# Performance work log

Measured on AMD Instinct MI355X. Metric: run time of the kernel, lower is better.

The kernel has to match this reference:

```python
import jax, jax.numpy as jnp
import numpy as np

N_IN, N_OUT, D_H = 128, 128, 1024
EPS = 1e-5

def _bn(x, g, b):
    # BatchNorm1d in training mode: per-batch mean / biased variance
    m = jnp.mean(x, axis=0)
    v = jnp.mean((x - m) ** 2, axis=0)
    return g * (x - m) / jnp.sqrt(v + EPS) + b

def setup_inputs() -> dict:
    key = jax.random.key(0)
    ks = jax.random.split(key, 16)
    d_comb = N_IN + D_H
    s1 = 1.0 / np.sqrt(d_comb)
    s2 = 1.0 / np.sqrt(D_H)
    return {
        "X": jax.random.normal(ks[0], (512, 256, N_IN), dtype=jnp.float32),
        "W_u": jax.random.uniform(ks[1], (D_H, d_comb), jnp.float32, -s1, s1),
        "b_u": jax.random.uniform(ks[2], (D_H,), jnp.float32, -s1, s1),
        "W_r": jax.random.uniform(ks[3], (D_H, d_comb), jnp.float32, -s1, s1),
        "b_r": jax.random.uniform(ks[4], (D_H,), jnp.float32, -s1, s1),
        "W_h": jax.random.uniform(ks[5], (D_H, d_comb), jnp.float32, -s1, s1),
        "b_h": jax.random.uniform(ks[6], (D_H,), jnp.float32, -s1, s1),
        "W_o": jax.random.uniform(ks[7], (N_OUT, D_H), jnp.float32, -s2, s2),
        "b_o": jax.random.uniform(ks[8], (N_OUT,), jnp.float32, -s2, s2),
        "g_u": jnp.ones((D_H,), jnp.float32), "be_u": jnp.zeros((D_H,), jnp.float32),
        "g_r": jnp.ones((D_H,), jnp.float32), "be_r": jnp.zeros((D_H,), jnp.float32),
        "g_h": jnp.ones((D_H,), jnp.float32), "be_h": jnp.zeros((D_H,), jnp.float32),
    }

def reference(X, W_u, b_u, W_r, b_r, W_h, b_h, W_o, b_o,
              g_u, be_u, g_r, be_r, g_h, be_h):
    # X: (B, S, n_inputs); dropout p=0 -> identity
    B = X.shape[0]
    Xs = jnp.transpose(X, (1, 0, 2))  # (S, B, n_in)

    def step(h, x):
        comb = jnp.concatenate([x, h], axis=-1)                 # (B, n_in+d_h)
        u = jax.nn.sigmoid(_bn(comb @ W_u.T + b_u, g_u, be_u))  # update gate
        r = jax.nn.sigmoid(_bn(comb @ W_r.T + b_r, g_r, be_r))  # reset gate
        comb2 = jnp.concatenate([x, r * h], axis=-1)
        c = jnp.tanh(_bn(comb2 @ W_h.T + b_h, g_h, be_h))       # candidate
        h_new = (1.0 - u) * c + u * h
        o = jnp.tanh(h_new @ W_o.T + b_o)
        return h_new, o

    h0 = jnp.zeros((B, D_H), dtype=X.dtype)
    _, out = jax.lax.scan(step, h0, Xs)      # out: (S, B, n_out)
    return jnp.transpose(out, (1, 0, 2))     # (B, S, n_out)
```

## Files before the change

### kernel.cpp

```cpp
#include <hip/hip_runtime.h>

#define BB   512
#define SS   256
#define NIN  128
#define DH   1024
#define DC   1152
#define NOUT 128
#define EPSV 1e-5f

typedef _Float16 f16;
typedef _Float16 f16x8 __attribute__((ext_vector_type(8)));
typedef _Float16 f16x4 __attribute__((ext_vector_type(4)));
typedef float    f32x4 __attribute__((ext_vector_type(4)));

__device__ __forceinline__ float sigmoid_(float x) { return 1.0f / (1.0f + __expf(-x)); }
__device__ __forceinline__ float tanh_(float x) {
    x = fminf(fmaxf(x, -15.0f), 15.0f);
    float e = __expf(2.0f * x);
    return (e - 1.0f) / (e + 1.0f);
}

__global__ void k_convert(const float* __restrict__ Wu, const float* __restrict__ Wr,
                          const float* __restrict__ Wh_, const float* __restrict__ Wo_,
                          f16* __restrict__ wur, f16* __restrict__ wh, f16* __restrict__ wo)
{
    const int stride = gridDim.x * blockDim.x;
    const int i0 = blockIdx.x * blockDim.x + threadIdx.x;
    for (int i = i0; i < 2048 * 1152 / 4; i += stride) {
        int base = i * 4;
        int n = base / 1152, k = base % 1152;
        const float* src = (n < 1024) ? (Wu + (size_t)n * 1152 + k) : (Wr + (size_t)(n - 1024) * 1152 + k);
        float4 v = *(const float4*)src;
        f16x4 o; o[0] = (f16)v.x; o[1] = (f16)v.y; o[2] = (f16)v.z; o[3] = (f16)v.w;
        *(f16x4*)(wur + base) = o;
    }
    for (int i = i0; i < 1024 * 1152 / 4; i += stride) {
        int base = i * 4;
        float4 v = *(const float4*)(Wh_ + base);
        f16x4 o; o[0] = (f16)v.x; o[1] = (f16)v.y; o[2] = (f16)v.z; o[3] = (f16)v.w;
        *(f16x4*)(wh + base) = o;
    }
    for (int i = i0; i < 128 * 1024 / 4; i += stride) {
        int base = i * 4;
        float4 v = *(const float4*)(Wo_ + base);
        f16x4 o; o[0] = (f16)v.x; o[1] = (f16)v.y; o[2] = (f16)v.z; o[3] = (f16)v.w;
        *(f16x4*)(wo + base) = o;
    }
}

__global__ void k_init(const float* __restrict__ X, f16* __restrict__ comb, float* __restrict__ h32,
                       float* __restrict__ ssum_ur, float* __restrict__ ssq_ur,
                       float* __restrict__ ssum_c, float* __restrict__ ssq_c)
{
    const int stride = gridDim.x * blockDim.x;
    const int i0 = blockIdx.x * blockDim.x + threadIdx.x;
    for (int i = i0; i < BB * DC / 4; i += stride) {
        int base = i * 4;
        int m = base / DC, k = base % DC;
        f16x4 o;
        if (k < NIN) {
            float4 v = *(const float4*)(X + (size_t)m * SS * NIN + k);
            o[0] = (f16)v.x; o[1] = (f16)v.y; o[2] = (f16)v.z; o[3] = (f16)v.w;
        } else {
            o[0] = (f16)0.f; o[1] = (f16)0.f; o[2] = (f16)0.f; o[3] = (f16)0.f;
        }
        *(f16x4*)(comb + base) = o;
    }
    for (int i = i0; i < BB * DH / 4; i += stride)
        *(float4*)(h32 + i * 4) = make_float4(0.f, 0.f, 0.f, 0.f);
    for (int i = i0; i < 2 * 2048; i += stride) { ssum_ur[i] = 0.f; ssq_ur[i] = 0.f; }
    for (int i = i0; i < 2 * 1024; i += stride) { ssum_c[i] = 0.f; ssq_c[i] = 0.f; }
}

template<int KT, bool OEPI>
__device__ __forceinline__ void gemm_job(
    const f16* __restrict__ A, int lda, const f16* __restrict__ Bm,
    float* __restrict__ C, int ldc,
    float* __restrict__ ssum, float* __restrict__ ssq,
    const float* __restrict__ bo, float* __restrict__ outp, int so,
    int m0, int n0, f16 (*As)[64][72], f16 (*Bs)[64][72])
{
    constexpr int KH = KT / 2;
    constexpr int NC = KH / 64;
    const int tid  = threadIdx.x;
    const int lane = tid & 63;
    const int wave = tid >> 6;
    const int g    = tid >> 8;
    const int sq   = wave & 3, wm = sq >> 1, wn = sq & 1;
    const int t    = tid & 255;
    const int r0   = t >> 3, kg = t & 7;

    const f16* Ap  = A  + (size_t)(m0 + r0) * lda + g * KH + kg * 8;
    const f16* Ap2 = Ap + (size_t)32 * lda;
    const f16* Bp  = Bm + (size_t)(n0 + r0) * KT + g * KH + kg * 8;
    const f16* Bp2 = Bp + (size_t)32 * KT;

    f32x4 acc[2][2] = {};
    f16x8 pa0 = *(const f16x8*)Ap;
    f16x8 pa1 = *(const f16x8*)Ap2;
    f16x8 pb0 = *(const f16x8*)Bp;
    f16x8 pb1 = *(const f16x8*)Bp2;

    for (int c = 0; c < NC; ++c) {
        *(f16x8*)&As[g][r0][kg * 8]      = pa0;
        *(f16x8*)&As[g][r0 + 32][kg * 8] = pa1;
        *(f16x8*)&Bs[g][r0][kg * 8]      = pb0;
        *(f16x8*)&Bs[g][r0 + 32][kg * 8] = pb1;
        __syncthreads();
        if (c + 1 < NC) {
            pa0 = *(const f16x8*)(Ap  + (c + 1) * 64);
            pa1 = *(const f16x8*)(Ap2 + (c + 1) * 64);
            pb0 = *(const f16x8*)(Bp  + (c + 1) * 64);
            pb1 = *(const f16x8*)(Bp2 + (c + 1) * 64);
        }
#pragma unroll
        for (int ks = 0; ks < 2; ++ks) {
            const int kofs = ks * 32 + (lane >> 4) * 8;
            f16x8 a0 = *(const f16x8*)&As[g][wm * 32 + (lane & 15)][kofs];
            f16x8 a1 = *(const f16x8*)&As[g][wm * 32 + 16 + (lane & 15)][kofs];
            f16x8 b0 = *(const f16x8*)&Bs[g][wn * 32 + (lane & 15)][kofs];
            f16x8 b1 = *(const f16x8*)&Bs[g][wn * 32 + 16 + (lane & 15)][kofs];
            acc[0][0] = __builtin_amdgcn_mfma_f32_16x16x32_f16(a0, b0, acc[0][0], 0, 0, 0);
            acc[0][1] = __builtin_amdgcn_mfma_f32_16x16x32_f16(a0, b1, acc[0][1], 0, 0, 0);
            acc[1][0] = __builtin_amdgcn_mfma_f32_16x16x32_f16(a1, b0, acc[1][0], 0, 0, 0);
            acc[1][1] = __builtin_amdgcn_mfma_f32_16x16x32_f16(a1, b1, acc[1][1], 0, 0, 0);
        }
        __syncthreads();
    }

    float* red = (float*)As;
    const int rbase = (sq * 64 + lane) * 20;
    if (g == 1) {
#pragma unroll
        for (int fm = 0; fm < 2; ++fm)
#pragma unroll
            for (int fn = 0; fn < 2; ++fn)
                *(f32x4*)&red[rbase + (fm * 2 + fn) * 4] = acc[fm][fn];
    }
    __syncthreads();
    if (g == 0) {
#pragma unroll
        for (int fm = 0; fm < 2; ++fm)
#pragma unroll
            for (int fn = 0; fn < 2; ++fn)
                acc[fm][fn] += *(const f32x4*)&red[rbase + (fm * 2 + fn) * 4];

#pragma unroll
        for (int fm = 0; fm < 2; ++fm) {
#pragma unroll
            for (int fn = 0; fn < 2; ++fn) {
                const int row = m0 + wm * 32 + fm * 16 + (lane >> 4) * 4;
                const int col = n0 + wn * 32 + fn * 16 + (lane & 15);
                if constexpr (OEPI) {
#pragma unroll
                    for (int i = 0; i < 4; ++i) {
                        float v = tanh_(acc[fm][fn][i] + bo[col]);
                        outp[(size_t)(row + i) * (SS * NOUT) + (size_t)so * NOUT + col] = v;
                    }
                } else {
#pragma unroll
                    for (int i = 0; i < 4; ++i)
                        C[(size_t)(row + i) * ldc + col] = acc[fm][fn][i];
                }
            }
        }
        if constexpr (!OEPI) {
#pragma unroll
            for (int fn = 0; fn < 2; ++fn) {
                float s1 = 0.f, s2 = 0.f;
#pragma unroll
                for (int fm = 0; fm < 2; ++fm)
#pragma unroll
                    for (int i = 0; i < 4; ++i) { float v = acc[fm][fn][i]; s1 += v; s2 += v * v; }
                s1 += __shfl_xor(s1, 16, 64); s1 += __shfl_xor(s1, 32, 64);
                s2 += __shfl_xor(s2, 16, 64); s2 += __shfl_xor(s2, 32, 64);
                if (lane < 16) {
                    const int col = n0 + wn * 32 + fn * 16 + lane;
                    atomicAdd(&ssum[col], s1);
                    atomicAdd(&ssq[col], s2);
                }
            }
        }
    }
}

__global__ __launch_bounds__(512, 4)
void k_uro(const f16* __restrict__ comb, const f16* __restrict__ Wur, const f16* __restrict__ Wo16,
           float* __restrict__ pre_ur,
           float* __restrict__ ssum, float* __restrict__ ssq,
           const float* __restrict__ b_o, float* __restrict__ outp, int s)
{
    __shared__ __align__(16) f16 smem[2][2][64][72];
    const int b = blockIdx.x;
    if (b < 16) {
        if (s == 0) return;
        const int m0 = (b >> 1) * 64, n0 = (b & 1) * 64;
        gemm_job<DH, true>(comb + NIN, DC, Wo16, nullptr, 0, nullptr, nullptr,
                           b_o, outp, s - 1, m0, n0, smem[0], smem[1]);
    } else {
        const int j = b - 16;
        const int m0 = (j >> 5) * 64, n0 = (j & 31) * 64;
        gemm_job<DC, false>(comb, DC, Wur, pre_ur, 2048, ssum, ssq,
                            nullptr, nullptr, 0, m0, n0, smem[0], smem[1]);
    }
}

__global__ __launch_bounds__(512, 4)
void k_c8(const f16* __restrict__ comb, const f16* __restrict__ Wh16,
          float* __restrict__ pre_c, float* __restrict__ ssum, float* __restrict__ ssq)
{
    __shared__ __align__(16) f16 smem[2][2][64][72];
    const int b = blockIdx.x;
    const int m0 = (b >> 4) * 64, n0 = (b & 15) * 64;
    gemm_job<DC, false>(comb, DC, Wh16, pre_c, 1024, ssum, ssq,
                        nullptr, nullptr, 0, m0, n0, smem[0], smem[1]);
}

__global__ __launch_bounds__(512, 4)
void k_o16(const f16* __restrict__ comb, const f16* __restrict__ Wo16,
           const float* __restrict__ b_o, float* __restrict__ outp)
{
    __shared__ __align__(16) f16 smem[2][2][64][72];
    const int b = blockIdx.x;
    const int m0 = (b >> 1) * 64, n0 = (b & 1) * 64;
    gemm_job<DH, true>(comb + NIN, DC, Wo16, nullptr, 0, nullptr, nullptr,
                       b_o, outp, SS - 1, m0, n0, smem[0], smem[1]);
}

__global__ __launch_bounds__(256)
void k_gate(const float* __restrict__ pre_ur, const float* __restrict__ h32,
            f16* __restrict__ comb,
            const float* __restrict__ ssum_ur, const float* __restrict__ ssq_ur,
            const float* __restrict__ g_r, const float* __restrict__ be_r)
{
    const int idx = blockIdx.x * 256 + threadIdx.x;
    const int m = idx >> 8, j4 = (idx & 255) << 2;
    float4 prv = *(const float4*)(pre_ur + (size_t)m * 2048 + 1024 + j4);
    float4 hv  = *(const float4*)(h32 + (size_t)m * 1024 + j4);
    float p[4] = {prv.x, prv.y, prv.z, prv.w};
    float h[4] = {hv.x, hv.y, hv.z, hv.w};
    f16x4 o;
#pragma unroll
    for (int t = 0; t < 4; ++t) {
        const int col = 1024 + j4 + t;
        float mu  = ssum_ur[col] * (1.0f / 512.0f);
        float var = fmaxf(ssq_ur[col] * (1.0f / 512.0f) - mu * mu, 0.f);
        float r   = sigmoid_(g_r[j4 + t] * ((p[t] - mu) * rsqrtf(var + EPSV)) + be_r[j4 + t]);
        o[t] = (f16)(r * h[t]);
    }
    *(f16x4*)(comb + (size_t)m * DC + NIN + j4) = o;
}

__global__ __launch_bounds__(256)
void k_upd(const float* __restrict__ pre_ur, const float* __restrict__ pre_c,
           float* __restrict__ h32, f16* __restrict__ comb,
           const float* __restrict__ ssum_ur, const float* __restrict__ ssq_ur,
           const float* __restrict__ ssum_c, const float* __restrict__ ssq_c,
           float* __restrict__ zsum_ur, float* __restrict__ zsq_ur,
           float* __restrict__ zsum_c, float* __restrict__ zsq_c,
           const float* __restrict__ X,
           const float* __restrict__ g_u, const float* __restrict__ be_u,
           const float* __restrict__ g_h, const float* __restrict__ be_h,
           int s)
{
    const int idx = blockIdx.x * 256 + threadIdx.x;
    const int m = idx >> 8, j4 = (idx & 255) << 2;
    float4 puv = *(const float4*)(pre_ur + (size_t)m * 2048 + j4);
    float4 pcv = *(const float4*)(pre_c + (size_t)m * 1024 + j4);
    float4 hv  = *(const float4*)(h32 + (size_t)m * 1024 + j4);
    float pu[4] = {puv.x, puv.y, puv.z, puv.w};
    float pc[4] = {pcv.x, pcv.y, pcv.z, pcv.w};
    float h[4]  = {hv.x, hv.y, hv.z, hv.w};
    float hn[4];
    f16x4 o;
#pragma unroll
    for (int t = 0; t < 4; ++t) {
        const int col = j4 + t;
        float mu_u  = ssum_ur[col] * (1.0f / 512.0f);
        float var_u = fmaxf(ssq_ur[col] * (1.0f / 512.0f) - mu_u * mu_u, 0.f);
        float u = sigmoid_(g_u[col] * ((pu[t] - mu_u) * rsqrtf(var_u + EPSV)) + be_u[col]);
        float mu_c  = ssum_c[col] * (1.0f / 512.0f);
        float var_c = fmaxf(ssq_c[col] * (1.0f / 512.0f) - mu_c * mu_c, 0.f);
        float c = tanh_(g_h[col] * ((pc[t] - mu_c) * rsqrtf(var_c + EPSV)) + be_h[col]);
        float hnew = (1.f - u) * c + u * h[t];
        hn[t] = hnew; o[t] = (f16)hnew;
    }
    *(float4*)(h32 + (size_t)m * 1024 + j4) = make_float4(hn[0], hn[1], hn[2], hn[3]);
    *(f16x4*)(comb + (size_t)m * DC + NIN + j4) = o;
    if (j4 < NIN && s + 1 < SS) {
        float4 xv = *(const float4*)(X + (size_t)m * SS * NIN + (size_t)(s + 1) * NIN + j4);
        f16x4 xo; xo[0] = (f16)xv.x; xo[1] = (f16)xv.y; xo[2] = (f16)xv.z; xo[3] = (f16)xv.w;
        *(f16x4*)(comb + (size_t)m * DC + j4) = xo;
    }
    if (idx < 2048) { zsum_ur[idx] = 0.f; zsq_ur[idx] = 0.f; }
    if (idx < 1024) { zsum_c[idx] = 0.f; zsq_c[idx] = 0.f; }
}

extern "C" void kernel_launch(void* const* d_in, const int* in_sizes, int n_in,
                              void* d_out, int out_size, void* d_ws, size_t ws_size,
                              hipStream_t stream)
{
    const float* X    = (const float*)d_in[0];
    const float* W_u  = (const float*)d_in[1];
    const float* W_r  = (const float*)d_in[3];
    const float* W_h  = (const float*)d_in[5];
    const float* W_o  = (const float*)d_in[7];
    const float* b_o  = (const float*)d_in[8];
    const float* g_u  = (const float*)d_in[9];
    const float* be_u = (const float*)d_in[10];
    const float* g_r  = (const float*)d_in[11];
    const float* be_r = (const float*)d_in[12];
    const float* g_h  = (const float*)d_in[13];
    const float* be_h = (const float*)d_in[14];
    float* out = (float*)d_out;

    char* p = (char*)d_ws;
    auto alloc = [&](size_t bytes) { char* r = p; p += (bytes + 255) & ~(size_t)255; return r; };
    f16*   comb    = (f16*)alloc((size_t)BB * DC * 2);
    f16*   Wur     = (f16*)alloc((size_t)2048 * DC * 2);
    f16*   Wh16    = (f16*)alloc((size_t)DH * DC * 2);
    f16*   Wo16    = (f16*)alloc((size_t)NOUT * DH * 2);
    float* pre_ur  = (float*)alloc((size_t)BB * 2048 * 4);
    float* pre_c   = (float*)alloc((size_t)BB * DH * 4);
    float* h32     = (float*)alloc((size_t)BB * DH * 4);
    float* ssum_ur = (float*)alloc(2 * 2048 * 4);
    float* ssq_ur  = (float*)alloc(2 * 2048 * 4);
    float* ssum_c  = (float*)alloc(2 * 1024 * 4);
    float* ssq_c   = (float*)alloc(2 * 1024 * 4);

    k_convert<<<1024, 256, 0, stream>>>(W_u, W_r, W_h, W_o, Wur, Wh16, Wo16);
    k_init<<<1024, 256, 0, stream>>>(X, comb, h32, ssum_ur, ssq_ur, ssum_c, ssq_c);

    for (int s = 0; s < SS; ++s) {
        const int par = s & 1, nxt = 1 - par;
        k_uro<<<272, 512, 0, stream>>>(comb, Wur, Wo16, pre_ur,
                                       ssum_ur + par * 2048, ssq_ur + par * 2048,
                                       b_o, out, s);
        k_gate<<<512, 256, 0, stream>>>(pre_ur, h32, comb,
            ssum_ur + par * 2048, ssq_ur + par * 2048, g_r, be_r);
        k_c8<<<128, 512, 0, stream>>>(comb, Wh16, pre_c,
                                      ssum_c + par * 1024, ssq_c + par * 1024);
        k_upd<<<512, 256, 0, stream>>>(pre_ur, pre_c, h32, comb,
            ssum_ur + par * 2048, ssq_ur + par * 2048,
            ssum_c + par * 1024, ssq_c + par * 1024,
            ssum_ur + nxt * 2048, ssq_ur + nxt * 2048,
            ssum_c + nxt * 1024, ssq_c + nxt * 1024,
            X, g_u, be_u, g_h, be_h, s);
    }
    k_o16<<<16, 512, 0, stream>>>(comb, Wo16, b_o, out);
}
```

Measured before the change: 8.055 ms.

## Fuse reset-gate computation into candidate GEMM A-tile loading and regroup kernels

Removes the separate reset-gate elementwise kernel. The candidate GEMM now builds its A operand on the fly from pre_ur, h32 and the BN statistics, computing sigmoid(r)*h directly into shared memory. The output projection moves from the update/reset GEMM launch into the candidate GEMM launch, and launch bounds drop from 4 to 2 blocks per CU. This saves one launch per timestep plus the f16 write and re-read of the gated half of comb. In exchange, each of the 16 column blocks recomputes the gate for its rows and reads fp32 pre_ur and h32 instead of f16, which adds redundant transcendental work and extra memory traffic.

```diff
diff --git a/kernel.cpp b/kernel.cpp
--- a/kernel.cpp
+++ b/kernel.cpp
@@ -184,39 +184,165 @@
     }
 }
 
-__global__ __launch_bounds__(512, 4)
-void k_uro(const f16* __restrict__ comb, const f16* __restrict__ Wur, const f16* __restrict__ Wo16,
-           float* __restrict__ pre_ur,
-           float* __restrict__ ssum, float* __restrict__ ssq,
-           const float* __restrict__ b_o, float* __restrict__ outp, int s)
+__device__ __forceinline__ void gemm_job_cgate(
+    const f16* __restrict__ comb, const float* __restrict__ pre_ur, const float* __restrict__ h32,
+    const float* __restrict__ su, const float* __restrict__ qu,
+    const float* __restrict__ g_r, const float* __restrict__ be_r,
+    const f16* __restrict__ Bm,
+    float* __restrict__ C, int ldc,
+    float* __restrict__ ssum, float* __restrict__ ssq,
+    int m0, int n0, f16 (*As)[64][72], f16 (*Bs)[64][72])
+{
+    constexpr int KT = DC, KH = KT / 2, NC = KH / 64;
+    const int tid  = threadIdx.x;
+    const int lane = tid & 63;
+    const int wave = tid >> 6;
+    const int g    = tid >> 8;
+    const int sq   = wave & 3, wm = sq >> 1, wn = sq & 1;
+    const int t    = tid & 255;
+    const int r0   = t >> 3, kg = t & 7;
+
+    const f16* Bp  = Bm + (size_t)(n0 + r0) * KT + g * KH + kg * 8;
+    const f16* Bp2 = Bp + (size_t)32 * KT;
+    const int kb   = g * KH + kg * 8;
+
+    f32x4 acc[2][2] = {};
+
+    for (int c = 0; c < NC; ++c) {
+        const int k8 = kb + c * 64;
+        f16x8 a0, a1;
+        if (k8 < NIN) {
+            a0 = *(const f16x8*)(comb + (size_t)(m0 + r0) * DC + k8);
+            a1 = *(const f16x8*)(comb + (size_t)(m0 + r0 + 32) * DC + k8);
+        } else {
+            const int j = k8 - NIN;
+            float sc[8], bi[8];
+#pragma unroll
+            for (int q = 0; q < 8; ++q) {
+                float mu  = su[1024 + j + q] * (1.0f / 512.0f);
+                float var = fmaxf(qu[1024 + j + q] * (1.0f / 512.0f) - mu * mu, 0.f);
+                float a   = g_r[j + q] * rsqrtf(var + EPSV);
+                sc[q] = a; bi[q] = be_r[j + q] - a * mu;
+            }
+            const float* pr0 = pre_ur + (size_t)(m0 + r0) * 2048 + 1024 + j;
+            const float* pr1 = pre_ur + (size_t)(m0 + r0 + 32) * 2048 + 1024 + j;
+            const float* hr0 = h32 + (size_t)(m0 + r0) * 1024 + j;
+            const float* hr1 = h32 + (size_t)(m0 + r0 + 32) * 1024 + j;
+            f32x4 p00 = *(const f32x4*)pr0, p01 = *(const f32x4*)(pr0 + 4);
+            f32x4 p10 = *(const f32x4*)pr1, p11 = *(const f32x4*)(pr1 + 4);
+            f32x4 h00 = *(const f32x4*)hr0, h01 = *(const f32x4*)(hr0 + 4);
+            f32x4 h10 = *(const f32x4*)hr1, h11 = *(const f32x4*)(hr1 + 4);
+#pragma unroll
+            for (int q = 0; q < 4; ++q) {
+                a0[q]     = (f16)(sigmoid_(sc[q] * p00[q] + bi[q]) * h00[q]);
+                a0[q + 4] = (f16)(sigmoid_(sc[q + 4] * p01[q] + bi[q + 4]) * h01[q]);
+                a1[q]     = (f16)(sigmoid_(sc[q] * p10[q] + bi[q]) * h10[q]);
+                a1[q + 4] = (f16)(sigmoid_(sc[q + 4] * p11[q] + bi[q + 4]) * h11[q]);
+            }
+        }
+        f16x8 b0v = *(const f16x8*)(Bp  + c * 64);
+        f16x8 b1v = *(const f16x8*)(Bp2 + c * 64);
+        *(f16x8*)&As[g][r0][kg * 8]      = a0;
+        *(f16x8*)&As[g][r0 + 32][kg * 8] = a1;
+        *(f16x8*)&Bs[g][r0][kg * 8]      = b0v;
+        *(f16x8*)&Bs[g][r0 + 32][kg * 8] = b1v;
+        __syncthreads();
+#pragma unroll
+        for (int ks = 0; ks < 2; ++ks) {
+            const int kofs = ks * 32 + (lane >> 4) * 8;
+            f16x8 fa0 = *(const f16x8*)&As[g][wm * 32 + (lane & 15)][kofs];
+            f16x8 fa1 = *(const f16x8*)&As[g][wm * 32 + 16 + (lane & 15)][kofs];
+            f16x8 fb0 = *(const f16x8*)&Bs[g][wn * 32 + (lane & 15)][kofs];
+            f16x8 fb1 = *(const f16x8*)&Bs[g][wn * 32 + 16 + (lane & 15)][kofs];
+            acc[0][0] = __builtin_amdgcn_mfma_f32_16x16x32_f16(fa0, fb0, acc[0][0], 0, 0, 0);
+            acc[0][1] = __builtin_amdgcn_mfma_f32_16x16x32_f16(fa0, fb1, acc[0][1], 0, 0, 0);
+            acc[1][0] = __builtin_amdgcn_mfma_f32_16x16x32_f16(fa1, fb0, acc[1][0], 0, 0, 0);
+            acc[1][1] = __builtin_amdgcn_mfma_f32_16x16x32_f16(fa1, fb1, acc[1][1], 0, 0, 0);
+        }
+        __syncthreads();
+    }
+
+    float* red = (float*)As;
+    const int rbase = (sq * 64 + lane) * 20;
+    if (g == 1) {
+#pragma unroll
+        for (int fm = 0; fm < 2; ++fm)
+#pragma unroll
+            for (int fn = 0; fn < 2; ++fn)
+                *(f32x4*)&red[rbase + (fm * 2 + fn) * 4] = acc[fm][fn];
+    }
+    __syncthreads();
+    if (g == 0) {
+#pragma unroll
+        for (int fm = 0; fm < 2; ++fm)
+#pragma unroll
+            for (int fn = 0; fn < 2; ++fn)
+                acc[fm][fn] += *(const f32x4*)&red[rbase + (fm * 2 + fn) * 4];
+
+#pragma unroll
+        for (int fm = 0; fm < 2; ++fm)
+#pragma unroll
+            for (int fn = 0; fn < 2; ++fn) {
+                const int row = m0 + wm * 32 + fm * 16 + (lane >> 4) * 4;
+                const int col = n0 + wn * 32 + fn * 16 + (lane & 15);
+#pragma unroll
+                for (int i = 0; i < 4; ++i)
+                    C[(size_t)(row + i) * ldc + col] = acc[fm][fn][i];
+            }
+#pragma unroll
+        for (int fn = 0; fn < 2; ++fn) {
+            float s1 = 0.f, s2 = 0.f;
+#pragma unroll
+            for (int fm = 0; fm < 2; ++fm)
+#pragma unroll
+                for (int i = 0; i < 4; ++i) { float v = acc[fm][fn][i]; s1 += v; s2 += v * v; }
+            s1 += __shfl_xor(s1, 16, 64); s1 += __shfl_xor(s1, 32, 64);
+            s2 += __shfl_xor(s2, 16, 64); s2 += __shfl_xor(s2, 32, 64);
+            if (lane < 16) {
+                const int col = n0 + wn * 32 + fn * 16 + lane;
+                atomicAdd(&ssum[col], s1);
+                atomicAdd(&ssq[col], s2);
+            }
+        }
+    }
+}
+
+__global__ __launch_bounds__(512, 2)
+void k_ur(const f16* __restrict__ comb, const f16* __restrict__ Wur,
+          float* __restrict__ pre_ur, float* __restrict__ ssum, float* __restrict__ ssq)
 {
     __shared__ __align__(16) f16 smem[2][2][64][72];
     const int b = blockIdx.x;
-    if (b < 16) {
+    const int m0 = (b >> 5) * 64, n0 = (b & 31) * 64;
+    gemm_job<DC, false>(comb, DC, Wur, pre_ur, 2048, ssum, ssq,
+                        nullptr, nullptr, 0, m0, n0, smem[0], smem[1]);
+}
+
+__global__ __launch_bounds__(512, 2)
+void k_cgo(const f16* __restrict__ comb, const float* __restrict__ pre_ur, const float* __restrict__ h32,
+           const f16* __restrict__ Wh16, const f16* __restrict__ Wo16,
+           float* __restrict__ pre_c,
+           const float* __restrict__ su, const float* __restrict__ qu,
+           float* __restrict__ sc_, float* __restrict__ qc_,
+           const float* __restrict__ g_r, const float* __restrict__ be_r,
+           const float* __restrict__ b_o, float* __restrict__ outp, int s)
+{
+    __shared__ __align__(16) f16 smem[2][2][64][72];
+    const int b = blockIdx.x;
+    if (b < 128) {
+        const int m0 = (b >> 4) * 64, n0 = (b & 15) * 64;
+        gemm_job_cgate(comb, pre_ur, h32, su, qu, g_r, be_r, Wh16,
+                       pre_c, 1024, sc_, qc_, m0, n0, smem[0], smem[1]);
+    } else {
         if (s == 0) return;
-        const int m0 = (b >> 1) * 64, n0 = (b & 1) * 64;
+        const int j = b - 128;
+        const int m0 = (j >> 1) * 64, n0 = (j & 1) * 64;
         gemm_job<DH, true>(comb + NIN, DC, Wo16, nullptr, 0, nullptr, nullptr,
                            b_o, outp, s - 1, m0, n0, smem[0], smem[1]);
-    } else {
-        const int j = b - 16;
-        const int m0 = (j >> 5) * 64, n0 = (j & 31) * 64;
-        gemm_job<DC, false>(comb, DC, Wur, pre_ur, 2048, ssum, ssq,
-                            nullptr, nullptr, 0, m0, n0, smem[0], smem[1]);
-    }
-}
-
-__global__ __launch_bounds__(512, 4)
-void k_c8(const f16* __restrict__ comb, const f16* __restrict__ Wh16,
-          float* __restrict__ pre_c, float* __restrict__ ssum, float* __restrict__ ssq)
-{
-    __shared__ __align__(16) f16 smem[2][2][64][72];
-    const int b = blockIdx.x;
-    const int m0 = (b >> 4) * 64, n0 = (b & 15) * 64;
-    gemm_job<DC, false>(comb, DC, Wh16, pre_c, 1024, ssum, ssq,
-                        nullptr, nullptr, 0, m0, n0, smem[0], smem[1]);
-}
-
-__global__ __launch_bounds__(512, 4)
+    }
+}
+
+__global__ __launch_bounds__(512, 2)
 void k_o16(const f16* __restrict__ comb, const f16* __restrict__ Wo16,
            const float* __restrict__ b_o, float* __restrict__ outp)
 {
@@ -225,30 +351,6 @@
     const int m0 = (b >> 1) * 64, n0 = (b & 1) * 64;
     gemm_job<DH, true>(comb + NIN, DC, Wo16, nullptr, 0, nullptr, nullptr,
                        b_o, outp, SS - 1, m0, n0, smem[0], smem[1]);
-}
-
-__global__ __launch_bounds__(256)
-void k_gate(const float* __restrict__ pre_ur, const float* __restrict__ h32,
-            f16* __restrict__ comb,
-            const float* __restrict__ ssum_ur, const float* __restrict__ ssq_ur,
-            const float* __restrict__ g_r, const float* __restrict__ be_r)
-{
-    const int idx = blockIdx.x * 256 + threadIdx.x;
-    const int m = idx >> 8, j4 = (idx & 255) << 2;
-    float4 prv = *(const float4*)(pre_ur + (size_t)m * 2048 + 1024 + j4);
-    float4 hv  = *(const float4*)(h32 + (size_t)m * 1024 + j4);
-    float p[4] = {prv.x, prv.y, prv.z, prv.w};
-    float h[4] = {hv.x, hv.y, hv.z, hv.w};
-    f16x4 o;
-#pragma unroll
-    for (int t = 0; t < 4; ++t) {
-        const int col = 1024 + j4 + t;
-        float mu  = ssum_ur[col] * (1.0f / 512.0f);
-        float var = fmaxf(ssq_ur[col] * (1.0f / 512.0f) - mu * mu, 0.f);
-        float r   = sigmoid_(g_r[j4 + t] * ((p[t] - mu) * rsqrtf(var + EPSV)) + be_r[j4 + t]);
-        o[t] = (f16)(r * h[t]);
-    }
-    *(f16x4*)(comb + (size_t)m * DC + NIN + j4) = o;
 }
 
 __global__ __launch_bounds__(256)
@@ -333,13 +435,12 @@
 
     for (int s = 0; s < SS; ++s) {
         const int par = s & 1, nxt = 1 - par;
-        k_uro<<<272, 512, 0, stream>>>(comb, Wur, Wo16, pre_ur,
+        k_ur<<<256, 512, 0, stream>>>(comb, Wur, pre_ur,
+                                      ssum_ur + par * 2048, ssq_ur + par * 2048);
+        k_cgo<<<144, 512, 0, stream>>>(comb, pre_ur, h32, Wh16, Wo16, pre_c,
                                        ssum_ur + par * 2048, ssq_ur + par * 2048,
-                                       b_o, out, s);
-        k_gate<<<512, 256, 0, stream>>>(pre_ur, h32, comb,
-            ssum_ur + par * 2048, ssq_ur + par * 2048, g_r, be_r);
-        k_c8<<<128, 512, 0, stream>>>(comb, Wh16, pre_c,
-                                      ssum_c + par * 1024, ssq_c + par * 1024);
+                                       ssum_c + par * 1024, ssq_c + par * 1024,
+                                       g_r, be_r, b_o, out, s);
         k_upd<<<512, 256, 0, stream>>>(pre_ur, pre_c, h32, comb,
             ssum_ur + par * 2048, ssq_ur + par * 2048,
             ssum_c + par * 1024, ssq_c + par * 1024,
```

After: 10.52 ms. +30.6%, slower.

## Fuse gate and update elementwise kernels into GEMM tails via last-block counters

Applied to the files above, without the earlier changes.

Removes the separate k_gate and k_upd launches by having the last GEMM block finishing each 64-column group (detected with an atomic counter) apply the BatchNorm+activation epilogue for that column slice. The reset-gated hidden is written to a separate double-buffered comb buffer so the u/r/o GEMM and the candidate GEMM read consistent inputs. Per step this cuts kernel launches from four to two. In exchange it adds atomic counters, fences, and a serialized epilogue on one block per column group, and launch bounds drop to 2 waves per EU.

```diff
diff --git a/kernel.cpp b/kernel.cpp
--- a/kernel.cpp
+++ b/kernel.cpp
@@ -48,9 +48,11 @@
     }
 }
 
-__global__ void k_init(const float* __restrict__ X, f16* __restrict__ comb, float* __restrict__ h32,
+__global__ void k_init(const float* __restrict__ X, f16* __restrict__ combA, f16* __restrict__ combB,
+                       float* __restrict__ h32,
                        float* __restrict__ ssum_ur, float* __restrict__ ssq_ur,
-                       float* __restrict__ ssum_c, float* __restrict__ ssq_c)
+                       float* __restrict__ ssum_c, float* __restrict__ ssq_c,
+                       unsigned* __restrict__ urt, unsigned* __restrict__ ct)
 {
     const int stride = gridDim.x * blockDim.x;
     const int i0 = blockIdx.x * blockDim.x + threadIdx.x;
@@ -64,12 +66,16 @@
         } else {
             o[0] = (f16)0.f; o[1] = (f16)0.f; o[2] = (f16)0.f; o[3] = (f16)0.f;
         }
-        *(f16x4*)(comb + base) = o;
+        *(f16x4*)(combA + base) = o;
+        *(f16x4*)(combB + base) = o;
+        f16x4 z; z[0] = (f16)0.f; z[1] = (f16)0.f; z[2] = (f16)0.f; z[3] = (f16)0.f;
+        *(f16x4*)(combB + (size_t)BB * DC + base) = z;
     }
     for (int i = i0; i < BB * DH / 4; i += stride)
         *(float4*)(h32 + i * 4) = make_float4(0.f, 0.f, 0.f, 0.f);
     for (int i = i0; i < 2 * 2048; i += stride) { ssum_ur[i] = 0.f; ssq_ur[i] = 0.f; }
     for (int i = i0; i < 2 * 1024; i += stride) { ssum_c[i] = 0.f; ssq_c[i] = 0.f; }
+    for (int i = i0; i < 16; i += stride) { urt[i] = 0u; ct[i] = 0u; }
 }
 
 template<int KT, bool OEPI>
@@ -184,116 +190,152 @@
     }
 }
 
-__global__ __launch_bounds__(512, 4)
-void k_uro(const f16* __restrict__ comb, const f16* __restrict__ Wur, const f16* __restrict__ Wo16,
+__global__ __launch_bounds__(512, 2)
+void k_uro(const f16* __restrict__ combA, const f16* __restrict__ Wur, const f16* __restrict__ Wo16,
            float* __restrict__ pre_ur,
            float* __restrict__ ssum, float* __restrict__ ssq,
-           const float* __restrict__ b_o, float* __restrict__ outp, int s)
+           f16* __restrict__ combB_par, const float* __restrict__ h32,
+           const float* __restrict__ g_r, const float* __restrict__ be_r,
+           const float* __restrict__ b_o, float* __restrict__ outp,
+           unsigned* __restrict__ urt, int s)
 {
     __shared__ __align__(16) f16 smem[2][2][64][72];
+    __shared__ int lastFlag;
     const int b = blockIdx.x;
     if (b < 16) {
         if (s == 0) return;
         const int m0 = (b >> 1) * 64, n0 = (b & 1) * 64;
-        gemm_job<DH, true>(comb + NIN, DC, Wo16, nullptr, 0, nullptr, nullptr,
+        gemm_job<DH, true>(combA + NIN, DC, Wo16, nullptr, 0, nullptr, nullptr,
                            b_o, outp, s - 1, m0, n0, smem[0], smem[1]);
-    } else {
-        const int j = b - 16;
-        const int m0 = (j >> 5) * 64, n0 = (j & 31) * 64;
-        gemm_job<DC, false>(comb, DC, Wur, pre_ur, 2048, ssum, ssq,
-                            nullptr, nullptr, 0, m0, n0, smem[0], smem[1]);
-    }
-}
-
-__global__ __launch_bounds__(512, 4)
-void k_c8(const f16* __restrict__ comb, const f16* __restrict__ Wh16,
-          float* __restrict__ pre_c, float* __restrict__ ssum, float* __restrict__ ssq)
+        return;
+    }
+    const int j = b - 16;
+    const int m0 = (j >> 5) * 64, n0 = (j & 31) * 64;
+    gemm_job<DC, false>(combA, DC, Wur, pre_ur, 2048, ssum, ssq,
+                        nullptr, nullptr, 0, m0, n0, smem[0], smem[1]);
+    if (n0 < 1024) return;
+    const int gid = (n0 - 1024) >> 6;
+    __syncthreads();
+    if (threadIdx.x == 0) {
+        __threadfence();
+        unsigned n = __hip_atomic_fetch_add(&urt[gid], 1u, __ATOMIC_ACQ_REL, __HIP_MEMORY_SCOPE_AGENT);
+        lastFlag = (n == (unsigned)(s * 8 + 7));
+    }
+    __syncthreads();
+    if (!lastFlag) return;
+    __builtin_amdgcn_fence(__ATOMIC_ACQUIRE, "agent");
+
+    const int tid = threadIdx.x;
+    const int hc0 = n0 - 1024;
+    const int c4 = (tid & 15) * 4;
+    const int rb = tid >> 4;
+    float mu[4], rq[4], gg[4], bb[4];
+#pragma unroll
+    for (int q = 0; q < 4; ++q) {
+        const int col = n0 + c4 + q;
+        float m_ = ssum[col] * (1.0f / 512.0f);
+        float v_ = fmaxf(ssq[col] * (1.0f / 512.0f) - m_ * m_, 0.f);
+        mu[q] = m_; rq[q] = rsqrtf(v_ + EPSV);
+        gg[q] = g_r[hc0 + c4 + q]; bb[q] = be_r[hc0 + c4 + q];
+    }
+#pragma unroll 4
+    for (int rr = 0; rr < 16; ++rr) {
+        const int row = rb + rr * 32;
+        f32x4 p = *(const f32x4*)(pre_ur + (size_t)row * 2048 + n0 + c4);
+        f32x4 h = *(const f32x4*)(h32 + (size_t)row * 1024 + hc0 + c4);
+        f16x4 o;
+#pragma unroll
+        for (int q = 0; q < 4; ++q) {
+            float r = sigmoid_(gg[q] * ((p[q] - mu[q]) * rq[q]) + bb[q]);
+            o[q] = (f16)(r * h[q]);
+        }
+        *(f16x4*)(combB_par + (size_t)row * DC + NIN + hc0 + c4) = o;
+    }
+}
+
+__global__ __launch_bounds__(512, 2)
+void k_c(const f16* __restrict__ combB_par, const f16* __restrict__ Wh16,
+         float* __restrict__ pre_c, float* __restrict__ sc_, float* __restrict__ qc_,
+         const float* __restrict__ pre_ur,
+         const float* __restrict__ su, const float* __restrict__ qu,
+         float* __restrict__ h32, f16* __restrict__ combA, f16* __restrict__ combB_nxt,
+         float* __restrict__ z_su, float* __restrict__ z_qu,
+         float* __restrict__ z_sc, float* __restrict__ z_qc,
+         const float* __restrict__ X,
+         const float* __restrict__ g_u, const float* __restrict__ be_u,
+         const float* __restrict__ g_h, const float* __restrict__ be_h,
+         unsigned* __restrict__ ct, int s)
 {
     __shared__ __align__(16) f16 smem[2][2][64][72];
+    __shared__ int lastFlag;
     const int b = blockIdx.x;
     const int m0 = (b >> 4) * 64, n0 = (b & 15) * 64;
-    gemm_job<DC, false>(comb, DC, Wh16, pre_c, 1024, ssum, ssq,
+    gemm_job<DC, false>(combB_par, DC, Wh16, pre_c, 1024, sc_, qc_,
                         nullptr, nullptr, 0, m0, n0, smem[0], smem[1]);
-}
-
-__global__ __launch_bounds__(512, 4)
-void k_o16(const f16* __restrict__ comb, const f16* __restrict__ Wo16,
+    const int gid = n0 >> 6;
+    __syncthreads();
+    if (threadIdx.x == 0) {
+        __threadfence();
+        unsigned n = __hip_atomic_fetch_add(&ct[gid], 1u, __ATOMIC_ACQ_REL, __HIP_MEMORY_SCOPE_AGENT);
+        lastFlag = (n == (unsigned)(s * 8 + 7));
+    }
+    __syncthreads();
+    if (!lastFlag) return;
+    __builtin_amdgcn_fence(__ATOMIC_ACQUIRE, "agent");
+
+    const int tid = threadIdx.x;
+    const int c4 = (tid & 15) * 4;
+    const int rb = tid >> 4;
+    float muU[4], rqU[4], gU[4], bU[4], muC[4], rqC[4], gH[4], bH[4];
+#pragma unroll
+    for (int q = 0; q < 4; ++q) {
+        const int col = n0 + c4 + q;
+        float m1 = su[col] * (1.0f / 512.0f);
+        float v1 = fmaxf(qu[col] * (1.0f / 512.0f) - m1 * m1, 0.f);
+        muU[q] = m1; rqU[q] = rsqrtf(v1 + EPSV); gU[q] = g_u[col]; bU[q] = be_u[col];
+        float m2 = sc_[col] * (1.0f / 512.0f);
+        float v2 = fmaxf(qc_[col] * (1.0f / 512.0f) - m2 * m2, 0.f);
+        muC[q] = m2; rqC[q] = rsqrtf(v2 + EPSV); gH[q] = g_h[col]; bH[q] = be_h[col];
+    }
+    const bool doX = (n0 + c4 < NIN) && (s + 1 < SS);
+#pragma unroll 2
+    for (int rr = 0; rr < 16; ++rr) {
+        const int row = rb + rr * 32;
+        f32x4 pu = *(const f32x4*)(pre_ur + (size_t)row * 2048 + n0 + c4);
+        f32x4 pc = *(const f32x4*)(pre_c + (size_t)row * 1024 + n0 + c4);
+        f32x4 h  = *(const f32x4*)(h32 + (size_t)row * 1024 + n0 + c4);
+        f32x4 hn; f16x4 o;
+#pragma unroll
+        for (int q = 0; q < 4; ++q) {
+            float u = sigmoid_(gU[q] * ((pu[q] - muU[q]) * rqU[q]) + bU[q]);
+            float c = tanh_(gH[q] * ((pc[q] - muC[q]) * rqC[q]) + bH[q]);
+            float hv = (1.f - u) * c + u * h[q];
+            hn[q] = hv; o[q] = (f16)hv;
+        }
+        *(f32x4*)(h32 + (size_t)row * 1024 + n0 + c4) = hn;
+        *(f16x4*)(combA + (size_t)row * DC + NIN + n0 + c4) = o;
+        if (doX) {
+            f32x4 xv = *(const f32x4*)(X + (size_t)row * SS * NIN + (size_t)(s + 1) * NIN + n0 + c4);
+            f16x4 xo;
+#pragma unroll
+            for (int q = 0; q < 4; ++q) xo[q] = (f16)xv[q];
+            *(f16x4*)(combA + (size_t)row * DC + n0 + c4) = xo;
+            *(f16x4*)(combB_nxt + (size_t)row * DC + n0 + c4) = xo;
+        }
+    }
+    if (tid < 128) { z_su[gid * 128 + tid] = 0.f; z_qu[gid * 128 + tid] = 0.f; }
+    if (tid < 64)  { z_sc[gid * 64 + tid] = 0.f;  z_qc[gid * 64 + tid] = 0.f; }
+}
+
+__global__ __launch_bounds__(512, 2)
+void k_o16(const f16* __restrict__ combA, const f16* __restrict__ Wo16,
            const float* __restrict__ b_o, float* __restrict__ outp)
 {
     __shared__ __align__(16) f16 smem[2][2][64][72];
     const int b = blockIdx.x;
     const int m0 = (b >> 1) * 64, n0 = (b & 1) * 64;
-    gemm_job<DH, true>(comb + NIN, DC, Wo16, nullptr, 0, nullptr, nullptr,
+    gemm_job<DH, true>(combA + NIN, DC, Wo16, nullptr, 0, nullptr, nullptr,
                        b_o, outp, SS - 1, m0, n0, smem[0], smem[1]);
-}
-
-__global__ __launch_bounds__(256)
-void k_gate(const float* __restrict__ pre_ur, const float* __restrict__ h32,
-            f16* __restrict__ comb,
-            const float* __restrict__ ssum_ur, const float* __restrict__ ssq_ur,
-            const float* __restrict__ g_r, const float* __restrict__ be_r)
-{
-    const int idx = blockIdx.x * 256 + threadIdx.x;
-    const int m = idx >> 8, j4 = (idx & 255) << 2;
-    float4 prv = *(const float4*)(pre_ur + (size_t)m * 2048 + 1024 + j4);
-    float4 hv  = *(const float4*)(h32 + (size_t)m * 1024 + j4);
-    float p[4] = {prv.x, prv.y, prv.z, prv.w};
-    float h[4] = {hv.x, hv.y, hv.z, hv.w};
-    f16x4 o;
-#pragma unroll
-    for (int t = 0; t < 4; ++t) {
-        const int col = 1024 + j4 + t;
-        float mu  = ssum_ur[col] * (1.0f / 512.0f);
-        float var = fmaxf(ssq_ur[col] * (1.0f / 512.0f) - mu * mu, 0.f);
-        float r   = sigmoid_(g_r[j4 + t] * ((p[t] - mu) * rsqrtf(var + EPSV)) + be_r[j4 + t]);
-        o[t] = (f16)(r * h[t]);
-    }
-    *(f16x4*)(comb + (size_t)m * DC + NIN + j4) = o;
-}
-
-__global__ __launch_bounds__(256)
-void k_upd(const float* __restrict__ pre_ur, const float* __restrict__ pre_c,
-           float* __restrict__ h32, f16* __restrict__ comb,
-           const float* __restrict__ ssum_ur, const float* __restrict__ ssq_ur,
-           const float* __restrict__ ssum_c, const float* __restrict__ ssq_c,
-           float* __restrict__ zsum_ur, float* __restrict__ zsq_ur,
-           float* __restrict__ zsum_c, float* __restrict__ zsq_c,
-           const float* __restrict__ X,
-           const float* __restrict__ g_u, const float* __restrict__ be_u,
-           const float* __restrict__ g_h, const float* __restrict__ be_h,
-           int s)
-{
-    const int idx = blockIdx.x * 256 + threadIdx.x;
-    const int m = idx >> 8, j4 = (idx & 255) << 2;
-    float4 puv = *(const float4*)(pre_ur + (size_t)m * 2048 + j4);
-    float4 pcv = *(const float4*)(pre_c + (size_t)m * 1024 + j4);
-    float4 hv  = *(const float4*)(h32 + (size_t)m * 1024 + j4);
-    float pu[4] = {puv.x, puv.y, puv.z, puv.w};
-    float pc[4] = {pcv.x, pcv.y, pcv.z, pcv.w};
-    float h[4]  = {hv.x, hv.y, hv.z, hv.w};
-    float hn[4];
-    f16x4 o;
-#pragma unroll
-    for (int t = 0; t < 4; ++t) {
-        const int col = j4 + t;
-        float mu_u  = ssum_ur[col] * (1.0f / 512.0f);
-        float var_u = fmaxf(ssq_ur[col] * (1.0f / 512.0f) - mu_u * mu_u, 0.f);
-        float u = sigmoid_(g_u[col] * ((pu[t] - mu_u) * rsqrtf(var_u + EPSV)) + be_u[col]);
-        float mu_c  = ssum_c[col] * (1.0f / 512.0f);
-        float var_c = fmaxf(ssq_c[col] * (1.0f / 512.0f) - mu_c * mu_c, 0.f);
-        float c = tanh_(g_h[col] * ((pc[t] - mu_c) * rsqrtf(var_c + EPSV)) + be_h[col]);
-        float hnew = (1.f - u) * c + u * h[t];
-        hn[t] = hnew; o[t] = (f16)hnew;
-    }
-    *(float4*)(h32 + (size_t)m * 1024 + j4) = make_float4(hn[0], hn[1], hn[2], hn[3]);
-    *(f16x4*)(comb + (size_t)m * DC + NIN + j4) = o;
-    if (j4 < NIN && s + 1 < SS) {
-        float4 xv = *(const float4*)(X + (size_t)m * SS * NIN + (size_t)(s + 1) * NIN + j4);
-        f16x4 xo; xo[0] = (f16)xv.x; xo[1] = (f16)xv.y; xo[2] = (f16)xv.z; xo[3] = (f16)xv.w;
-        *(f16x4*)(comb + (size_t)m * DC + j4) = xo;
-    }
-    if (idx < 2048) { zsum_ur[idx] = 0.f; zsq_ur[idx] = 0.f; }
-    if (idx < 1024) { zsum_c[idx] = 0.f; zsq_c[idx] = 0.f; }
 }
 
 extern "C" void kernel_launch(void* const* d_in, const int* in_sizes, int n_in,
@@ -316,7 +358,8 @@
 
     char* p = (char*)d_ws;
     auto alloc = [&](size_t bytes) { char* r = p; p += (bytes + 255) & ~(size_t)255; return r; };
-    f16*   comb    = (f16*)alloc((size_t)BB * DC * 2);
+    f16*   combA   = (f16*)alloc((size_t)BB * DC * 2);
+    f16*   combB   = (f16*)alloc((size_t)2 * BB * DC * 2);
     f16*   Wur     = (f16*)alloc((size_t)2048 * DC * 2);
     f16*   Wh16    = (f16*)alloc((size_t)DH * DC * 2);
     f16*   Wo16    = (f16*)alloc((size_t)NOUT * DH * 2);
@@ -327,25 +370,26 @@
     float* ssq_ur  = (float*)alloc(2 * 2048 * 4);
     float* ssum_c  = (float*)alloc(2 * 1024 * 4);
     float* ssq_c   = (float*)alloc(2 * 1024 * 4);
+    unsigned* urt  = (unsigned*)alloc(16 * 4);
+    unsigned* ct   = (unsigned*)alloc(16 * 4);
 
     k_convert<<<1024, 256, 0, stream>>>(W_u, W_r, W_h, W_o, Wur, Wh16, Wo16);
-    k_init<<<1024, 256, 0, stream>>>(X, comb, h32, ssum_ur, ssq_ur, ssum_c, ssq_c);
+    k_init<<<1024, 256, 0, stream>>>(X, combA, combB, h32,
+                                     ssum_ur, ssq_ur, ssum_c, ssq_c, urt, ct);
 
     for (int s = 0; s < SS; ++s) {
         const int par = s & 1, nxt = 1 - par;
-        k_uro<<<272, 512, 0, stream>>>(comb, Wur, Wo16, pre_ur,
+        k_uro<<<272, 512, 0, stream>>>(combA, Wur, Wo16, pre_ur,
                                        ssum_ur + par * 2048, ssq_ur + par * 2048,
-                                       b_o, out, s);
-        k_gate<<<512, 256, 0, stream>>>(pre_ur, h32, comb,
-            ssum_ur + par * 2048, ssq_ur + par * 2048, g_r, be_r);
-        k_c8<<<128, 512, 0, stream>>>(comb, Wh16, pre_c,
-                                      ssum_c + par * 1024, ssq_c + par * 1024);
-        k_upd<<<512, 256, 0, stream>>>(pre_ur, pre_c, h32, comb,
-            ssum_ur + par * 2048, ssq_ur + par * 2048,
-            ssum_c + par * 1024, ssq_c + par * 1024,
-            ssum_ur + nxt * 2048, ssq_ur + nxt * 2048,
-            ssum_c + nxt * 1024, ssq_c + nxt * 1024,
-            X, g_u, be_u, g_h, be_h, s);
-    }
-    k_o16<<<16, 512, 0, stream>>>(comb, Wo16, b_o, out);
-}
+                                       combB + (size_t)par * BB * DC, h32,
+                                       g_r, be_r, b_o, out, urt, s);
+        k_c<<<128, 512, 0, stream>>>(combB + (size_t)par * BB * DC, Wh16,
+                                     pre_c, ssum_c + par * 1024, ssq_c + par * 1024,
+                                     pre_ur, ssum_ur + par * 2048, ssq_ur + par * 2048,
+                                     h32, combA, combB + (size_t)nxt * BB * DC,
+                                     ssum_ur + nxt * 2048, ssq_ur + nxt * 2048,
+                                     ssum_c + nxt * 1024, ssq_c + nxt * 1024,
+                                     X, g_u, be_u, g_h, be_h, ct, s);
+    }
+    k_o16<<<16, 512, 0, stream>>>(combA, Wo16, b_o, out);
+}
```

Measured after the change: 17.42 ms. 116% more time.

## Double-buffer comb, move output GEMM into candidate kernel, deepen register prefetch

Applied to the files above, without the earlier changes.

Splits the combined input buffer in two: combA holds [x, h] and combB holds [x, r*h]. This lets the output projection of the previous step read combA while the candidate GEMM reads combB. The output GEMM moves from the update/reset kernel into the candidate kernel, which balances block counts (256 and 144 blocks). The GEMM inner loop now prefetches global tiles two chunks ahead into registers, and launch bounds drop from 4 to 2 blocks per CU. Costs include more registers, extra writes of x into both buffers, and lower occupancy.

```diff
diff --git a/kernel.cpp b/kernel.cpp
--- a/kernel.cpp
+++ b/kernel.cpp
@@ -48,7 +48,8 @@
     }
 }
 
-__global__ void k_init(const float* __restrict__ X, f16* __restrict__ comb, float* __restrict__ h32,
+__global__ void k_init(const float* __restrict__ X, f16* __restrict__ combA, f16* __restrict__ combB,
+                       float* __restrict__ h32,
                        float* __restrict__ ssum_ur, float* __restrict__ ssq_ur,
                        float* __restrict__ ssum_c, float* __restrict__ ssq_c)
 {
@@ -64,7 +65,8 @@
         } else {
             o[0] = (f16)0.f; o[1] = (f16)0.f; o[2] = (f16)0.f; o[3] = (f16)0.f;
         }
-        *(f16x4*)(comb + base) = o;
+        *(f16x4*)(combA + base) = o;
+        *(f16x4*)(combB + base) = o;
     }
     for (int i = i0; i < BB * DH / 4; i += stride)
         *(float4*)(h32 + i * 4) = make_float4(0.f, 0.f, 0.f, 0.f);
@@ -96,22 +98,24 @@
     const f16* Bp2 = Bp + (size_t)32 * KT;
 
     f32x4 acc[2][2] = {};
-    f16x8 pa0 = *(const f16x8*)Ap;
-    f16x8 pa1 = *(const f16x8*)Ap2;
-    f16x8 pb0 = *(const f16x8*)Bp;
-    f16x8 pb1 = *(const f16x8*)Bp2;
+    f16x8 ra0[2], ra1[2], rb0[2], rb1[2];
+    ra0[0] = *(const f16x8*)Ap;          ra1[0] = *(const f16x8*)Ap2;
+    rb0[0] = *(const f16x8*)Bp;          rb1[0] = *(const f16x8*)Bp2;
+    ra0[1] = *(const f16x8*)(Ap + 64);   ra1[1] = *(const f16x8*)(Ap2 + 64);
+    rb0[1] = *(const f16x8*)(Bp + 64);   rb1[1] = *(const f16x8*)(Bp2 + 64);
 
     for (int c = 0; c < NC; ++c) {
-        *(f16x8*)&As[g][r0][kg * 8]      = pa0;
-        *(f16x8*)&As[g][r0 + 32][kg * 8] = pa1;
-        *(f16x8*)&Bs[g][r0][kg * 8]      = pb0;
-        *(f16x8*)&Bs[g][r0 + 32][kg * 8] = pb1;
+        const int cur = c & 1;
+        *(f16x8*)&As[g][r0][kg * 8]      = ra0[cur];
+        *(f16x8*)&As[g][r0 + 32][kg * 8] = ra1[cur];
+        *(f16x8*)&Bs[g][r0][kg * 8]      = rb0[cur];
+        *(f16x8*)&Bs[g][r0 + 32][kg * 8] = rb1[cur];
         __syncthreads();
-        if (c + 1 < NC) {
-            pa0 = *(const f16x8*)(Ap  + (c + 1) * 64);
-            pa1 = *(const f16x8*)(Ap2 + (c + 1) * 64);
-            pb0 = *(const f16x8*)(Bp  + (c + 1) * 64);
-            pb1 = *(const f16x8*)(Bp2 + (c + 1) * 64);
+        if (c + 2 < NC) {
+            ra0[cur] = *(const f16x8*)(Ap  + (c + 2) * 64);
+            ra1[cur] = *(const f16x8*)(Ap2 + (c + 2) * 64);
+            rb0[cur] = *(const f16x8*)(Bp  + (c + 2) * 64);
+            rb1[cur] = *(const f16x8*)(Bp2 + (c + 2) * 64);
         }
 #pragma unroll
         for (int ks = 0; ks < 2; ++ks) {
@@ -184,52 +188,20 @@
     }
 }
 
-__global__ __launch_bounds__(512, 4)
-void k_uro(const f16* __restrict__ comb, const f16* __restrict__ Wur, const f16* __restrict__ Wo16,
-           float* __restrict__ pre_ur,
-           float* __restrict__ ssum, float* __restrict__ ssq,
-           const float* __restrict__ b_o, float* __restrict__ outp, int s)
+__global__ __launch_bounds__(512, 2)
+void k_ur(const f16* __restrict__ combA, const f16* __restrict__ Wur,
+          float* __restrict__ pre_ur, float* __restrict__ ssum, float* __restrict__ ssq)
 {
     __shared__ __align__(16) f16 smem[2][2][64][72];
     const int b = blockIdx.x;
-    if (b < 16) {
-        if (s == 0) return;
-        const int m0 = (b >> 1) * 64, n0 = (b & 1) * 64;
-        gemm_job<DH, true>(comb + NIN, DC, Wo16, nullptr, 0, nullptr, nullptr,
-                           b_o, outp, s - 1, m0, n0, smem[0], smem[1]);
-    } else {
-        const int j = b - 16;
-        const int m0 = (j >> 5) * 64, n0 = (j & 31) * 64;
-        gemm_job<DC, false>(comb, DC, Wur, pre_ur, 2048, ssum, ssq,
-                            nullptr, nullptr, 0, m0, n0, smem[0], smem[1]);
-    }
-}
-
-__global__ __launch_bounds__(512, 4)
-void k_c8(const f16* __restrict__ comb, const f16* __restrict__ Wh16,
-          float* __restrict__ pre_c, float* __restrict__ ssum, float* __restrict__ ssq)
-{
-    __shared__ __align__(16) f16 smem[2][2][64][72];
-    const int b = blockIdx.x;
-    const int m0 = (b >> 4) * 64, n0 = (b & 15) * 64;
-    gemm_job<DC, false>(comb, DC, Wh16, pre_c, 1024, ssum, ssq,
+    const int m0 = (b >> 5) * 64, n0 = (b & 31) * 64;
+    gemm_job<DC, false>(combA, DC, Wur, pre_ur, 2048, ssum, ssq,
                         nullptr, nullptr, 0, m0, n0, smem[0], smem[1]);
-}
-
-__global__ __launch_bounds__(512, 4)
-void k_o16(const f16* __restrict__ comb, const f16* __restrict__ Wo16,
-           const float* __restrict__ b_o, float* __restrict__ outp)
-{
-    __shared__ __align__(16) f16 smem[2][2][64][72];
-    const int b = blockIdx.x;
-    const int m0 = (b >> 1) * 64, n0 = (b & 1) * 64;
-    gemm_job<DH, true>(comb + NIN, DC, Wo16, nullptr, 0, nullptr, nullptr,
-                       b_o, outp, SS - 1, m0, n0, smem[0], smem[1]);
 }
 
 __global__ __launch_bounds__(256)
 void k_gate(const float* __restrict__ pre_ur, const float* __restrict__ h32,
-            f16* __restrict__ comb,
+            f16* __restrict__ combB,
             const float* __restrict__ ssum_ur, const float* __restrict__ ssq_ur,
             const float* __restrict__ g_r, const float* __restrict__ be_r)
 {
@@ -248,12 +220,44 @@
         float r   = sigmoid_(g_r[j4 + t] * ((p[t] - mu) * rsqrtf(var + EPSV)) + be_r[j4 + t]);
         o[t] = (f16)(r * h[t]);
     }
-    *(f16x4*)(comb + (size_t)m * DC + NIN + j4) = o;
+    *(f16x4*)(combB + (size_t)m * DC + NIN + j4) = o;
+}
+
+__global__ __launch_bounds__(512, 2)
+void k_co(const f16* __restrict__ combB, const f16* __restrict__ combA,
+          const f16* __restrict__ Wh16, const f16* __restrict__ Wo16,
+          float* __restrict__ pre_c, float* __restrict__ ssum, float* __restrict__ ssq,
+          const float* __restrict__ b_o, float* __restrict__ outp, int s)
+{
+    __shared__ __align__(16) f16 smem[2][2][64][72];
+    const int b = blockIdx.x;
+    if (b < 128) {
+        const int m0 = (b >> 4) * 64, n0 = (b & 15) * 64;
+        gemm_job<DC, false>(combB, DC, Wh16, pre_c, 1024, ssum, ssq,
+                            nullptr, nullptr, 0, m0, n0, smem[0], smem[1]);
+    } else {
+        if (s == 0) return;
+        const int j = b - 128;
+        const int m0 = (j >> 1) * 64, n0 = (j & 1) * 64;
+        gemm_job<DH, true>(combA + NIN, DC, Wo16, nullptr, 0, nullptr, nullptr,
+                           b_o, outp, s - 1, m0, n0, smem[0], smem[1]);
+    }
+}
+
+__global__ __launch_bounds__(512, 2)
+void k_o16(const f16* __restrict__ combA, const f16* __restrict__ Wo16,
+           const float* __restrict__ b_o, float* __restrict__ outp)
+{
+    __shared__ __align__(16) f16 smem[2][2][64][72];
+    const int b = blockIdx.x;
+    const int m0 = (b >> 1) * 64, n0 = (b & 1) * 64;
+    gemm_job<DH, true>(combA + NIN, DC, Wo16, nullptr, 0, nullptr, nullptr,
+                       b_o, outp, SS - 1, m0, n0, smem[0], smem[1]);
 }
 
 __global__ __launch_bounds__(256)
 void k_upd(const float* __restrict__ pre_ur, const float* __restrict__ pre_c,
-           float* __restrict__ h32, f16* __restrict__ comb,
+           float* __restrict__ h32, f16* __restrict__ combA, f16* __restrict__ combB,
            const float* __restrict__ ssum_ur, const float* __restrict__ ssq_ur,
            const float* __restrict__ ssum_c, const float* __restrict__ ssq_c,
            float* __restrict__ zsum_ur, float* __restrict__ zsq_ur,
@@ -286,11 +290,12 @@
         hn[t] = hnew; o[t] = (f16)hnew;
     }
     *(float4*)(h32 + (size_t)m * 1024 + j4) = make_float4(hn[0], hn[1], hn[2], hn[3]);
-    *(f16x4*)(comb + (size_t)m * DC + NIN + j4) = o;
+    *(f16x4*)(combA + (size_t)m * DC + NIN + j4) = o;
     if (j4 < NIN && s + 1 < SS) {
         float4 xv = *(const float4*)(X + (size_t)m * SS * NIN + (size_t)(s + 1) * NIN + j4);
         f16x4 xo; xo[0] = (f16)xv.x; xo[1] = (f16)xv.y; xo[2] = (f16)xv.z; xo[3] = (f16)xv.w;
-        *(f16x4*)(comb + (size_t)m * DC + j4) = xo;
+        *(f16x4*)(combA + (size_t)m * DC + j4) = xo;
+        *(f16x4*)(combB + (size_t)m * DC + j4) = xo;
     }
     if (idx < 2048) { zsum_ur[idx] = 0.f; zsq_ur[idx] = 0.f; }
     if (idx < 1024) { zsum_c[idx] = 0.f; zsq_c[idx] = 0.f; }
@@ -316,7 +321,8 @@
 
     char* p = (char*)d_ws;
     auto alloc = [&](size_t bytes) { char* r = p; p += (bytes + 255) & ~(size_t)255; return r; };
-    f16*   comb    = (f16*)alloc((size_t)BB * DC * 2);
+    f16*   combA   = (f16*)alloc((size_t)BB * DC * 2);
+    f16*   combB   = (f16*)alloc((size_t)BB * DC * 2);
     f16*   Wur     = (f16*)alloc((size_t)2048 * DC * 2);
     f16*   Wh16    = (f16*)alloc((size_t)DH * DC * 2);
     f16*   Wo16    = (f16*)alloc((size_t)NOUT * DH * 2);
@@ -329,23 +335,23 @@
     float* ssq_c   = (float*)alloc(2 * 1024 * 4);
 
     k_convert<<<1024, 256, 0, stream>>>(W_u, W_r, W_h, W_o, Wur, Wh16, Wo16);
-    k_init<<<1024, 256, 0, stream>>>(X, comb, h32, ssum_ur, ssq_ur, ssum_c, ssq_c);
+    k_init<<<1024, 256, 0, stream>>>(X, combA, combB, h32, ssum_ur, ssq_ur, ssum_c, ssq_c);
 
     for (int s = 0; s < SS; ++s) {
         const int par = s & 1, nxt = 1 - par;
-        k_uro<<<272, 512, 0, stream>>>(comb, Wur, Wo16, pre_ur,
-                                       ssum_ur + par * 2048, ssq_ur + par * 2048,
-                                       b_o, out, s);
-        k_gate<<<512, 256, 0, stream>>>(pre_ur, h32, comb,
+        k_ur<<<256, 512, 0, stream>>>(combA, Wur, pre_ur,
+                                      ssum_ur + par * 2048, ssq_ur + par * 2048);
+        k_gate<<<512, 256, 0, stream>>>(pre_ur, h32, combB,
             ssum_ur + par * 2048, ssq_ur + par * 2048, g_r, be_r);
-        k_c8<<<128, 512, 0, stream>>>(comb, Wh16, pre_c,
-                                      ssum_c + par * 1024, ssq_c + par * 1024);
-        k_upd<<<512, 256, 0, stream>>>(pre_ur, pre_c, h32, comb,
+        k_co<<<144, 512, 0, stream>>>(combB, combA, Wh16, Wo16, pre_c,
+                                      ssum_c + par * 1024, ssq_c + par * 1024,
+                                      b_o, out, s);
+        k_upd<<<512, 256, 0, stream>>>(pre_ur, pre_c, h32, combA, combB,
             ssum_ur + par * 2048, ssq_ur + par * 2048,
             ssum_c + par * 1024, ssq_c + par * 1024,
             ssum_ur + nxt * 2048, ssq_ur + nxt * 2048,
             ssum_c + nxt * 1024, ssq_c + nxt * 1024,
             X, g_u, be_u, g_h, be_h, s);
     }
-    k_o16<<<16, 512, 0, stream>>>(comb, Wo16, b_o, out);
-}
+    k_o16<<<16, 512, 0, stream>>>(combA, Wo16, b_o, out);
+}
```

Result: slower. 25.19 ms (+212.7%).
